# Performance work log

Hardware: AMD Instinct MI355X
Metric: run time of the kernel (lower is better)

Reference implementation:

```python
import jax, jax.numpy as jnp
import numpy as np

BATCH, INPUTDIM, OUTDIM, GRIDSIZE = 4096, 256, 256, 64


def setup_inputs() -> dict:
    key = jax.random.key(0)
    k1, k2 = jax.random.split(key)
    x = jax.random.normal(k1, (BATCH, INPUTDIM), dtype=jnp.float32)
    # xavier_uniform over (2, outdim, inputdim, gridsize): fan_in = inputdim*gridsize, fan_out = outdim*gridsize
    fan_in = INPUTDIM * GRIDSIZE
    fan_out = OUTDIM * GRIDSIZE
    limit = float(np.sqrt(6.0 / (fan_in + fan_out)))
    fouriercoeffs = jax.random.uniform(
        k2, (2, OUTDIM, INPUTDIM, GRIDSIZE), dtype=jnp.float32,
        minval=-limit, maxval=limit)
    bias = jnp.zeros((1, OUTDIM), dtype=jnp.float32)
    return {"x": x, "fouriercoeffs": fouriercoeffs, "bias": bias}


def reference(x, fouriercoeffs, bias):
    # x: [B, inputdim]; fouriercoeffs: [2, outdim, inputdim, gridsize]; bias: [1, outdim]
    # gridsize_param is clamp/round'ed to an int in torch -> static = initial_gridsize here.
    G = fouriercoeffs.shape[-1]
    k = jnp.arange(1, G + 1, dtype=x.dtype)        # [G] frequencies 1..G
    xk = x[:, :, None] * k                          # [B, inputdim, G]
    c = jnp.cos(xk)                                 # [B, inputdim, G]
    s = jnp.sin(xk)                                 # [B, inputdim, G]
    # Fused contraction over (inputdim, gridsize) -- avoids the naive
    # [B, outdim, inputdim, gridsize] broadcast tensor of the torch code.
    y = (jnp.einsum('big,oig->bo', c, fouriercoeffs[0])
         + jnp.einsum('big,oig->bo', s, fouriercoeffs[1])
         + bias)                                    # [B, outdim]
    return y
```

## Files before the change

kernel.cpp:

```cpp
#include <hip/hip_runtime.h>
#include <hip/hip_bf16.h>


typedef __attribute__((ext_vector_type(8))) short short8;
typedef __attribute__((ext_vector_type(4))) float f32x4;

#define SPLITK 16
#define ICHUNK (256 / SPLITK)

#define INV2PI 0.15915494309189535f

__device__ __forceinline__ unsigned short f2bf(float f) {
    unsigned u = __builtin_bit_cast(unsigned, f);
    u += 0x7fffu + ((u >> 16) & 1u);
    return (unsigned short)(u >> 16);
}
#if __has_builtin(__builtin_amdgcn_cvt_pk_bf16_f32)
typedef __attribute__((ext_vector_type(2))) __bf16 bf16x2_t;
__device__ __forceinline__ unsigned pkbf16(float a, float b) {
    bf16x2_t v = __builtin_amdgcn_cvt_pk_bf16_f32(a, b);
    return __builtin_bit_cast(unsigned, v);
}
#else
__device__ __forceinline__ unsigned pkbf16(float a, float b) {
    unsigned ua = __builtin_bit_cast(unsigned, a) + 0x8000u;
    unsigned ub = __builtin_bit_cast(unsigned, b) + 0x8000u;
    return __builtin_amdgcn_perm(ub, ua, 0x07060302u);
}
#endif

__device__ __forceinline__ void dbl2(float c, float s, float& co, float& so) {
    float t = c + c;
    co = __builtin_fmaf(t, c, -1.f);
    so = t * s;
}
__device__ __forceinline__ void rot2(float c, float s, float cr, float sr,
                                     float& co, float& so) {
    float t = s * sr;
    co = __builtin_fmaf(c, cr, -t);
    float u = s * cr;
    so = __builtin_fmaf(c, sr, u);
}

__device__ __forceinline__ short8 chain8(float m1, float fm1, float f0) {
    unsigned r[4];
    float vp = fm1, v = f0;
    #pragma unroll
    for (int h = 0; h < 4; ++h) {
        float v1 = __builtin_fmaf(m1, v, -vp);
        r[h] = pkbf16(v, v1);
        float v2 = __builtin_fmaf(m1, v1, -v);
        vp = v1; v = v2;
    }
    uint4 u; u.x = r[0]; u.y = r[1]; u.z = r[2]; u.w = r[3];
    return __builtin_bit_cast(short8, u);
}

__device__ __forceinline__ void async_load16(const void* g, void* l) {
    __builtin_amdgcn_global_load_lds(
        (const __attribute__((address_space(1))) unsigned int*)g,
        (__attribute__((address_space(3))) unsigned int*)l,
        16, 0, 0);
}

__global__ __launch_bounds__(256) void prep_kernel(
    const float* __restrict__ fc, const float* __restrict__ bias,
    unsigned short* __restrict__ ws2, float* __restrict__ out, int base)
{
    const unsigned bid = blockIdx.x + base;
    const unsigned t = threadIdx.x;
    if (bid < 4096) {
        unsigned flat = bid * 256 + t;
        unsigned bx = flat >> 11, gi = flat & 2047;
        unsigned i = bx >> 1, y = bx & 1;
        unsigned sog = gi >> 6, ll = gi & 63;
        unsigned s = sog >> 3, og = sog & 7;
        unsigned op = og * 16 + (ll & 15);
        unsigned k = s * 32 + ((ll >> 4) * 8);
        unsigned tt = k >> 6, g0 = k & 63;
        const float4* src = (const float4*)(fc +
            ((((size_t)tt * 256 + y * 128 + op) * 256 + i) * 64 + g0));
        float4 a = src[0], b = src[1];
        uint4 v;
        v.x = pkbf16(a.x, a.y); v.y = pkbf16(a.z, a.w);
        v.z = pkbf16(b.x, b.y); v.w = pkbf16(b.z, b.w);
        ((uint4*)ws2)[flat] = v;
    } else {
        int tid = (bid - 4096) * 256 + t;
        float4 b4 = ((const float4*)bias)[tid & 63];
        ((float4*)out)[tid] = b4;
    }
}

__global__ __launch_bounds__(256) void reduce_kernel(
    const unsigned short* __restrict__ pws, const float* __restrict__ bias,
    float* __restrict__ out)
{
    int idx4 = blockIdx.x * 256 + threadIdx.x;
    float4 r = ((const float4*)bias)[idx4 & 63];
    #pragma unroll
    for (int z = 0; z < SPLITK; ++z) {
        ushort4 v = ((const ushort4*)pws)[(size_t)z * 262144 + idx4];
        r.x += __builtin_bit_cast(float, (unsigned)v.x << 16);
        r.y += __builtin_bit_cast(float, (unsigned)v.y << 16);
        r.z += __builtin_bit_cast(float, (unsigned)v.z << 16);
        r.w += __builtin_bit_cast(float, (unsigned)v.w << 16);
    }
    ((float4*)out)[idx4] = r;
}

template <bool USE_WS, bool PARTIAL>
__global__ __launch_bounds__(512, 2) void fkan_gemm(
    const float* __restrict__ x, const float* __restrict__ fc,
    const unsigned short* __restrict__ bws, float* __restrict__ out,
    unsigned short* __restrict__ pws)
{
    __shared__ uint4 Bimg[2][2048];
    __shared__ float xs[ICHUNK][512];

    const int t  = threadIdx.x;
    const int l  = t & 63;
    const int w  = t >> 6;
    const int q  = l >> 4;
    const int m  = l & 15;

    const int bid = blockIdx.x;
    const int z   = bid & 15;
    const int by  = (bid >> 4) & 1;
    const int bx  = bid >> 5;
    const int rowBase = bx * 512;
    const int iBase   = z * ICHUNK;

    f32x4 acc[4][8];
    #pragma unroll
    for (int a = 0; a < 4; ++a)
        #pragma unroll
        for (int b = 0; b < 8; ++b) acc[a][b] = (f32x4)0.0f;

    auto stageB = [&](int p, int i) {
        if (USE_WS) {
            const uint4* base = (const uint4*)bws + (size_t)(i * 2 + by) * 2048;
            #pragma unroll
            for (int cc = 0; cc < 4; ++cc) {
                int c = cc * 8 + w;
                async_load16(base + (size_t)c * 64 + l, (void*)(&Bimg[p][c * 64]));
            }
        } else {
            #pragma unroll
            for (int gg = 0; gg < 4; ++gg) {
                int gi  = gg * 512 + t;
                int sog = gi >> 6, ll = gi & 63;
                int s = sog >> 3, ogb = sog & 7;
                int o = ogb * 16 + (ll & 15);
                int k = s * 32 + (ll >> 4) * 8;
                int tt = k >> 6, g = k & 63;
                const float4* p4 = (const float4*)(fc +
                    ((((size_t)tt * 256 + by * 128 + o) * 256 + i) * 64 + g));
                float4 a = p4[0], b = p4[1];
                uint4 v;
                v.x = pkbf16(a.x, a.y); v.y = pkbf16(a.z, a.w);
                v.z = pkbf16(b.x, b.y); v.w = pkbf16(b.z, b.w);
                Bimg[p][gi] = v;
            }
        }
    };

    stageB(0, iBase);
    {
        const float4* px = (const float4*)(x + (size_t)(rowBase + t) * 256 + iBase);
        #pragma unroll
        for (int j4 = 0; j4 < 4; ++j4) {
            float4 v = px[j4];
            xs[j4 * 4 + 0][t] = v.x;
            xs[j4 * 4 + 1][t] = v.y;
            xs[j4 * 4 + 2][t] = v.z;
            xs[j4 * 4 + 3][t] = v.w;
        }
    }
    __syncthreads();

    #pragma unroll 1
    for (int ii = 0; ii < ICHUNK; ++ii) {
        const int p = ii & 1;

        if (ii + 1 < ICHUNK) stageB(p ^ 1, iBase + ii + 1);

        short8 aF[4][4];
        #pragma unroll
        for (int rf = 0; rf < 4; ++rf) {
            float xv = xs[ii][w * 64 + rf * 16 + m];
            float rev = xv * INV2PI;
            float s1 = __builtin_amdgcn_sinf(rev);
            float c1 = __builtin_amdgcn_cosf(rev);
            const float m1 = c1 + c1;
            float c2, s2, c4, s4, c8, s8, c16, s16, c32, s32;
            dbl2(c1, s1, c2, s2);
            dbl2(c2, s2, c4, s4);
            dbl2(c4, s4, c8, s8);
            dbl2(c8, s8, c16, s16);
            dbl2(c16, s16, c32, s32);
            float c24, s24;
            rot2(c16, s16, c8, s8, c24, s24);
            float cq = (q == 0) ? 1.f : (q == 1) ? c8 : (q == 2) ? c16 : c24;
            float sq = (q == 0) ? 0.f : (q == 1) ? s8 : (q == 2) ? s16 : s24;
            float cq1, sq1, cB, sB, cB1, sB1;
            rot2(cq, sq, c1, s1, cq1, sq1);
            rot2(cq, sq, c32, s32, cB, sB);
            rot2(cB, sB, c1, s1, cB1, sB1);
            aF[rf][0] = chain8(m1, cq, cq1);
            aF[rf][1] = chain8(m1, cB, cB1);
            aF[rf][2] = chain8(m1, sq, sq1);
            aF[rf][3] = chain8(m1, sB, sB1);
        }

        #pragma unroll
        for (int s = 0; s < 4; ++s) {
            short8 bF[8];
            #pragma unroll
            for (int cf = 0; cf < 8; ++cf)
                bF[cf] = __builtin_bit_cast(short8, Bimg[p][(s * 8 + cf) * 64 + l]);
            #pragma unroll
            for (int rf = 0; rf < 4; ++rf)
                #pragma unroll
                for (int cf = 0; cf < 8; ++cf)
                    acc[rf][cf] = __builtin_amdgcn_mfma_f32_16x16x32_bf16(
                        aF[rf][s], bF[cf], acc[rf][cf], 0, 0, 0);
        }

        __syncthreads();
    }

    const int r0 = rowBase + w * 64 + (l >> 4) * 4;
    const int c0 = by * 128 + m;
    if (PARTIAL) {
        unsigned short* dst = pws + (size_t)z * (4096u * 256u);
        #pragma unroll
        for (int rf = 0; rf < 4; ++rf)
            #pragma unroll
            for (int cf = 0; cf < 8; ++cf)
                #pragma unroll
                for (int e = 0; e < 4; ++e)
                    dst[(size_t)(r0 + rf * 16 + e) * 256 + (c0 + cf * 16)] =
                        f2bf(acc[rf][cf][e]);
    } else {
        #pragma unroll
        for (int rf = 0; rf < 4; ++rf)
            #pragma unroll
            for (int cf = 0; cf < 8; ++cf)
                #pragma unroll
                for (int e = 0; e < 4; ++e)
                    atomicAdd(out + (size_t)(r0 + rf * 16 + e) * 256 + (c0 + cf * 16),
                              acc[rf][cf][e]);
    }
}

extern "C" void kernel_launch(void* const* d_in, const int* in_sizes, int n_in,
                              void* d_out, int out_size, void* d_ws, size_t ws_size,
                              hipStream_t stream) {
    const float* x    = (const float*)d_in[0];
    const float* fc   = (const float*)d_in[1];
    const float* bias = (const float*)d_in[2];
    float* out = (float*)d_out;
    unsigned short* bws = (unsigned short*)d_ws;

    const size_t wsCoeff = (size_t)512 * 2048 * 16;
    const size_t wsFull  = wsCoeff + (size_t)SPLITK * 4096 * 256 * 2;
    unsigned short* pws = (unsigned short*)((char*)d_ws + wsCoeff);

    if (ws_size >= wsFull) {
        hipLaunchKernelGGL(prep_kernel, dim3(4096), dim3(256), 0, stream,
                           fc, bias, bws, out, 0);
        hipLaunchKernelGGL((fkan_gemm<true, true>), dim3(256), dim3(512), 0, stream,
                           x, fc, bws, out, pws);
        hipLaunchKernelGGL(reduce_kernel, dim3(1024), dim3(256), 0, stream,
                           pws, bias, out);
    } else if (ws_size >= wsCoeff) {
        hipLaunchKernelGGL(prep_kernel, dim3(5120), dim3(256), 0, stream,
                           fc, bias, bws, out, 0);
        hipLaunchKernelGGL((fkan_gemm<true, false>), dim3(256), dim3(512), 0, stream,
                           x, fc, bws, out, pws);
    } else {
        hipLaunchKernelGGL(prep_kernel, dim3(1024), dim3(256), 0, stream,
                           fc, bias, bws, out, 4096);
        hipLaunchKernelGGL((fkan_gemm<false, false>), dim3(256), dim3(512), 0, stream,
                           x, fc, bws, out, pws);
    }
}
```

Before: 151.3 us.

## Software-pipeline Fourier seed computation and build A fragments per k-step

```diff
diff --git a/kernel.cpp b/kernel.cpp
--- a/kernel.cpp
+++ b/kernel.cpp
@@ -62,6 +62,10 @@
         (__attribute__((address_space(3))) unsigned int*)l,
         16, 0, 0);
 }
+
+struct Seed {
+    float m1, cq, sq, c1, s1, c32, s32;
+};
 
 __global__ __launch_bounds__(256) void prep_kernel(
     const float* __restrict__ fc, const float* __restrict__ bias,
@@ -165,27 +169,7 @@
         }
     };
 
-    stageB(0, iBase);
-    {
-        const float4* px = (const float4*)(x + (size_t)(rowBase + t) * 256 + iBase);
-        #pragma unroll
-        for (int j4 = 0; j4 < 4; ++j4) {
-            float4 v = px[j4];
-            xs[j4 * 4 + 0][t] = v.x;
-            xs[j4 * 4 + 1][t] = v.y;
-            xs[j4 * 4 + 2][t] = v.z;
-            xs[j4 * 4 + 3][t] = v.w;
-        }
-    }
-    __syncthreads();
-
-    #pragma unroll 1
-    for (int ii = 0; ii < ICHUNK; ++ii) {
-        const int p = ii & 1;
-
-        if (ii + 1 < ICHUNK) stageB(p ^ 1, iBase + ii + 1);
-
-        short8 aF[4][4];
+    auto computeSeeds = [&](int ii, Seed sd[4]) {
         #pragma unroll
         for (int rf = 0; rf < 4; ++rf) {
             float xv = xs[ii][w * 64 + rf * 16 + m];
@@ -203,30 +187,97 @@
             rot2(c16, s16, c8, s8, c24, s24);
             float cq = (q == 0) ? 1.f : (q == 1) ? c8 : (q == 2) ? c16 : c24;
             float sq = (q == 0) ? 0.f : (q == 1) ? s8 : (q == 2) ? s16 : s24;
-            float cq1, sq1, cB, sB, cB1, sB1;
-            rot2(cq, sq, c1, s1, cq1, sq1);
-            rot2(cq, sq, c32, s32, cB, sB);
-            rot2(cB, sB, c1, s1, cB1, sB1);
-            aF[rf][0] = chain8(m1, cq, cq1);
-            aF[rf][1] = chain8(m1, cB, cB1);
-            aF[rf][2] = chain8(m1, sq, sq1);
-            aF[rf][3] = chain8(m1, sB, sB1);
-        }
-
-        #pragma unroll
-        for (int s = 0; s < 4; ++s) {
+            sd[rf].m1 = m1; sd[rf].cq = cq; sd[rf].sq = sq;
+            sd[rf].c1 = c1; sd[rf].s1 = s1;
+            sd[rf].c32 = c32; sd[rf].s32 = s32;
+        }
+    };
+
+    auto makeA = [&](const Seed& sd, int s) -> short8 {
+        float fm1, f0;
+        if (s == 0) {
+            fm1 = sd.cq;
+            f0  = __builtin_fmaf(sd.cq, sd.c1, -(sd.sq * sd.s1));
+        } else if (s == 1) {
+            float cB, sB;
+            rot2(sd.cq, sd.sq, sd.c32, sd.s32, cB, sB);
+            fm1 = cB;
+            f0  = __builtin_fmaf(cB, sd.c1, -(sB * sd.s1));
+        } else if (s == 2) {
+            fm1 = sd.sq;
+            f0  = __builtin_fmaf(sd.cq, sd.s1, sd.sq * sd.c1);
+        } else {
+            float cB, sB;
+            rot2(sd.cq, sd.sq, sd.c32, sd.s32, cB, sB);
+            fm1 = sB;
+            f0  = __builtin_fmaf(cB, sd.s1, sB * sd.c1);
+        }
+        return chain8(sd.m1, fm1, f0);
+    };
+
+    stageB(0, iBase);
+    {
+        const float4* px = (const float4*)(x + (size_t)(rowBase + t) * 256 + iBase);
+        #pragma unroll
+        for (int j4 = 0; j4 < 4; ++j4) {
+            float4 v = px[j4];
+            xs[j4 * 4 + 0][t] = v.x;
+            xs[j4 * 4 + 1][t] = v.y;
+            xs[j4 * 4 + 2][t] = v.z;
+            xs[j4 * 4 + 3][t] = v.w;
+        }
+    }
+    __syncthreads();
+
+    Seed sdC[4], sdN[4];
+    computeSeeds(0, sdC);
+
+    #pragma unroll 1
+    for (int ii = 0; ii < ICHUNK; ++ii) {
+        const int p = ii & 1;
+
+        if (ii + 1 < ICHUNK) stageB(p ^ 1, iBase + ii + 1);
+
+        {
             short8 bF[8];
             #pragma unroll
             for (int cf = 0; cf < 8; ++cf)
-                bF[cf] = __builtin_bit_cast(short8, Bimg[p][(s * 8 + cf) * 64 + l]);
+                bF[cf] = __builtin_bit_cast(short8, Bimg[p][(0 * 8 + cf) * 64 + l]);
+            short8 aF[4];
+            #pragma unroll
+            for (int rf = 0; rf < 4; ++rf) aF[rf] = makeA(sdC[rf], 0);
             #pragma unroll
             for (int rf = 0; rf < 4; ++rf)
                 #pragma unroll
                 for (int cf = 0; cf < 8; ++cf)
                     acc[rf][cf] = __builtin_amdgcn_mfma_f32_16x16x32_bf16(
-                        aF[rf][s], bF[cf], acc[rf][cf], 0, 0, 0);
-        }
-
+                        aF[rf], bF[cf], acc[rf][cf], 0, 0, 0);
+        }
+
+        {
+            int nxt = (ii + 1 < ICHUNK) ? ii + 1 : ii;
+            computeSeeds(nxt, sdN);
+        }
+
+        #pragma unroll
+        for (int s = 1; s < 4; ++s) {
+            short8 bF[8];
+            #pragma unroll
+            for (int cf = 0; cf < 8; ++cf)
+                bF[cf] = __builtin_bit_cast(short8, Bimg[p][(s * 8 + cf) * 64 + l]);
+            short8 aF[4];
+            #pragma unroll
+            for (int rf = 0; rf < 4; ++rf) aF[rf] = makeA(sdC[rf], s);
+            #pragma unroll
+            for (int rf = 0; rf < 4; ++rf)
+                #pragma unroll
+                for (int cf = 0; cf < 8; ++cf)
+                    acc[rf][cf] = __builtin_amdgcn_mfma_f32_16x16x32_bf16(
+                        aF[rf], bF[cf], acc[rf][cf], 0, 0, 0);
+        }
+
+        #pragma unroll
+        for (int rf = 0; rf < 4; ++rf) sdC[rf] = sdN[rf];
         __syncthreads();
     }
 
```

After: 154.3 us. No clear change (+2.0%).
